# Performance work log

Measured on AMD Instinct MI355X. Metric: run time of the kernel, lower is better.

## Reference

```python
import jax, jax.numpy as jnp
import numpy as np

N = 50000   # nodes
E = 800000  # edges (avg degree 16)
D = 128     # feature dim (in_feats and all hidden_feats)
L = 3       # number of SAGEConv layers


def setup_inputs() -> dict:
    key = jax.random.key(0)
    ks = jax.random.split(key, 3 + 3 * L)
    node_feats = jax.random.normal(ks[0], (N, D), dtype=jnp.float32)
    src = jax.random.randint(ks[1], (E,), 0, N)
    dst = jax.random.randint(ks[2], (E,), 0, N)
    inp = {"node_feats": node_feats, "src": src, "dst": dst}
    scale = 1.0 / np.sqrt(D)
    for i in range(L):
        inp[f"W_self{i}"] = (jax.random.normal(ks[3 + 3 * i], (D, D), dtype=jnp.float32) * scale)
        inp[f"W_neigh{i}"] = (jax.random.normal(ks[4 + 3 * i], (D, D), dtype=jnp.float32) * scale)
        inp[f"b{i}"] = jnp.zeros((D,), dtype=jnp.float32)
    return inp


def _sage_stack(node_feats, src, dst, layers):
    n = node_feats.shape[0]
    # in-degree per destination node, clamped so isolated nodes yield 0 aggregate
    deg = jax.ops.segment_sum(jnp.ones((src.shape[0],), dtype=node_feats.dtype), dst, num_segments=n)
    inv_deg = (1.0 / jnp.maximum(deg, 1.0))[:, None]  # [N,1]
    h = node_feats
    for (W_s, W_n, b) in layers:
        # gather neighbor feats along edges, mean-reduce into dst nodes
        agg = jax.ops.segment_sum(h[src], dst, num_segments=n) * inv_deg  # [N,D]
        # DGL SAGEConv ('mean'): fc_self(h_dst) + fc_neigh(mean_neigh) + bias, then activation
        h = jax.nn.relu(h @ W_s.T + agg @ W_n.T + b)
    return h


def reference(node_feats, src, dst, W_self0, W_neigh0, b0, W_self1, W_neigh1, b1, W_self2, W_neigh2, b2):
    layers = ((W_self0, W_neigh0, b0), (W_self1, W_neigh1, b1), (W_self2, W_neigh2, b2))
    return _sage_stack(node_feats, src, dst, layers)
```

## Files before the change

kernel.cpp:

```cpp
#include <hip/hip_runtime.h>
#include <hip/hip_bf16.h>

#define NN 50000
#define NE 800000
#define DF 128
#define NSL 128
#define SLN 391
#define CAP 8192
#define ECHUNK 1563

typedef __bf16 bf16x8 __attribute__((ext_vector_type(8)));
typedef float f32x4 __attribute__((ext_vector_type(4)));

__device__ __forceinline__ unsigned short f32_to_bf16_rne(float f) {
    unsigned int u = __float_as_uint(f);
    u += 0x7fffu + ((u >> 16) & 1u);
    return (unsigned short)(u >> 16);
}

__device__ __forceinline__ unsigned int pack_bf16x2(float lo, float hi) {
    return (unsigned int)f32_to_bf16_rne(lo) | ((unsigned int)f32_to_bf16_rne(hi) << 16);
}

__global__ __launch_bounds__(256) void k_bucket(const int* __restrict__ src, const int* __restrict__ dst,
                                                int* __restrict__ gcur, uint2* __restrict__ bucket) {
    __shared__ int cnt[NSL];
    __shared__ int rb[NSL];
    int t = threadIdx.x;
    for (int j = t; j < NSL; j += 256) cnt[j] = 0;
    __syncthreads();
    int base = blockIdx.x * ECHUNK;
    int end = base + ECHUNK;
    if (end > NE) end = NE;
    for (int i = base + t; i < end; i += 256) atomicAdd(&cnt[dst[i] / SLN], 1);
    __syncthreads();
    for (int j = t; j < NSL; j += 256) rb[j] = atomicAdd(&gcur[j], cnt[j]);
    __syncthreads();
    for (int j = t; j < NSL; j += 256) cnt[j] = rb[j];
    __syncthreads();
    for (int i = base + t; i < end; i += 256) {
        int d = dst[i];
        int s = d / SLN;
        int pos = atomicAdd(&cnt[s], 1);
        bucket[s * CAP + pos] = make_uint2((unsigned)src[i], (unsigned)d);
    }
}

__global__ void k_sbase(const int* __restrict__ gcur, int* __restrict__ sbase, int* __restrict__ row_ptr) {
    if (threadIdx.x == 0) {
        int acc = 0;
        for (int s = 0; s < NSL; ++s) {
            sbase[s] = acc;
            acc += gcur[s];
        }
        row_ptr[NN] = acc;
    }
}

__global__ __launch_bounds__(256) void k_cslice(const uint2* __restrict__ bucket, const int* __restrict__ gcur,
                                                const int* __restrict__ sbase, int* __restrict__ col,
                                                int* __restrict__ row_ptr, float* __restrict__ inv_deg) {
    __shared__ int sdeg[512];
    __shared__ int scur[512];
    int s = blockIdx.x;
    int t = threadIdx.x;
    int nbase = s * SLN;
    int ncnt = NN - nbase;
    if (ncnt > SLN) ncnt = SLN;
    int ecnt = gcur[s];
    int eb = s * CAP;
    int cb = sbase[s];
    sdeg[t] = 0;
    sdeg[t + 256] = 0;
    __syncthreads();
    for (int e = t; e < ecnt; e += 256) atomicAdd(&sdeg[bucket[eb + e].y - nbase], 1);
    __syncthreads();
    int d0 = sdeg[t], d1 = sdeg[t + 256];
    for (int off = 1; off < 512; off <<= 1) {
        int v0 = (t >= off) ? sdeg[t - off] : 0;
        int v1 = (t + 256 >= off) ? sdeg[t + 256 - off] : 0;
        __syncthreads();
        sdeg[t] += v0;
        sdeg[t + 256] += v1;
        __syncthreads();
    }
    int e0 = sdeg[t] - d0, e1 = sdeg[t + 256] - d1;
    scur[t] = e0;
    scur[t + 256] = e1;
    if (t < ncnt) {
        row_ptr[nbase + t] = cb + e0;
        inv_deg[nbase + t] = 1.0f / (float)(d0 > 1 ? d0 : 1);
    }
    if (t + 256 < ncnt) {
        row_ptr[nbase + t + 256] = cb + e1;
        inv_deg[nbase + t + 256] = 1.0f / (float)(d1 > 1 ? d1 : 1);
    }
    __syncthreads();
    for (int e = t; e < ecnt; e += 256) {
        uint2 pr = bucket[eb + e];
        int p = atomicAdd(&scur[pr.y - nbase], 1);
        col[cb + p] = (int)pr.x;
    }
}

__global__ __launch_bounds__(256) void k_f2b_all(const float* __restrict__ feats,
                                                 const float* __restrict__ w0, const float* __restrict__ w1,
                                                 const float* __restrict__ w2, const float* __restrict__ w3,
                                                 const float* __restrict__ w4, const float* __restrict__ w5,
                                                 unsigned short* __restrict__ h_bf,
                                                 unsigned short* __restrict__ Wb) {
    int i = (blockIdx.x * 256 + threadIdx.x) * 4;
    const float* fsrc;
    unsigned short* dstp;
    if (i < NN * DF) {
        fsrc = feats + i;
        dstp = h_bf + i;
    } else {
        int j = i - NN * DF;
        if (j >= 6 * DF * DF) return;
        int w = j >> 14;
        int o = j & 16383;
        const float* ws[6] = {w0, w1, w2, w3, w4, w5};
        fsrc = ws[w] + o;
        dstp = Wb + w * DF * DF + o;
    }
    float4 v = *reinterpret_cast<const float4*>(fsrc);
    ushort4 r;
    r.x = f32_to_bf16_rne(v.x);
    r.y = f32_to_bf16_rne(v.y);
    r.z = f32_to_bf16_rne(v.z);
    r.w = f32_to_bf16_rne(v.w);
    *reinterpret_cast<ushort4*>(dstp) = r;
}

__global__ __launch_bounds__(256) void k_agg(const unsigned short* __restrict__ H,
                                             const int* __restrict__ row_ptr, const int* __restrict__ col,
                                             const float* __restrict__ inv_deg,
                                             unsigned short* __restrict__ Agg, int n) {
    int wid = threadIdx.x >> 6;
    int lane = threadIdx.x & 63;
    int node = blockIdx.x * 4 + wid;
    if (node >= n) return;
    int s = row_ptr[node], e = row_ptr[node + 1];
    int g = lane >> 4;
    int l = lane & 15;
    int off = l * 8;

    float a[8];
#pragma unroll
    for (int k = 0; k < 8; ++k) a[k] = 0.f;

    for (int j = s; j < e; j += 8) {
        int j0 = j + g;
        int j1 = j + 4 + g;
        if (j0 < e) {
            int c = col[j0];
            uint4 u = *reinterpret_cast<const uint4*>(H + (size_t)c * DF + off);
            a[0] += __uint_as_float(u.x << 16);
            a[1] += __uint_as_float(u.x & 0xffff0000u);
            a[2] += __uint_as_float(u.y << 16);
            a[3] += __uint_as_float(u.y & 0xffff0000u);
            a[4] += __uint_as_float(u.z << 16);
            a[5] += __uint_as_float(u.z & 0xffff0000u);
            a[6] += __uint_as_float(u.w << 16);
            a[7] += __uint_as_float(u.w & 0xffff0000u);
        }
        if (j1 < e) {
            int c = col[j1];
            uint4 u = *reinterpret_cast<const uint4*>(H + (size_t)c * DF + off);
            a[0] += __uint_as_float(u.x << 16);
            a[1] += __uint_as_float(u.x & 0xffff0000u);
            a[2] += __uint_as_float(u.y << 16);
            a[3] += __uint_as_float(u.y & 0xffff0000u);
            a[4] += __uint_as_float(u.z << 16);
            a[5] += __uint_as_float(u.z & 0xffff0000u);
            a[6] += __uint_as_float(u.w << 16);
            a[7] += __uint_as_float(u.w & 0xffff0000u);
        }
    }

#pragma unroll
    for (int k = 0; k < 8; ++k) {
        a[k] += __shfl_xor(a[k], 16, 64);
        a[k] += __shfl_xor(a[k], 32, 64);
    }

    if (g == 0) {
        float iv = inv_deg[node];
        uint4 r;
        r.x = pack_bf16x2(a[0] * iv, a[1] * iv);
        r.y = pack_bf16x2(a[2] * iv, a[3] * iv);
        r.z = pack_bf16x2(a[4] * iv, a[5] * iv);
        r.w = pack_bf16x2(a[6] * iv, a[7] * iv);
        *reinterpret_cast<uint4*>(Agg + (size_t)node * DF + off) = r;
    }
}

__global__ __launch_bounds__(256) void k_gemm(const unsigned short* __restrict__ Hb,
                                              const unsigned short* __restrict__ Ab,
                                              const unsigned short* __restrict__ Wb,
                                              const float* __restrict__ bias,
                                              unsigned short* __restrict__ Hout,
                                              float* __restrict__ Fout,
                                              int n) {
    int brow = blockIdx.x * 64;
    int lane = threadIdx.x & 63;
    int wid = threadIdx.x >> 6;
    int l15 = lane & 15;
    int lk = (lane >> 4) * 8;
    int colb = wid * 32;

    f32x4 zero = {0.f, 0.f, 0.f, 0.f};
    f32x4 acc[4][2];
#pragma unroll
    for (int m = 0; m < 4; ++m) {
        acc[m][0] = zero;
        acc[m][1] = zero;
    }

#pragma unroll
    for (int ph = 0; ph < 2; ++ph) {
        const unsigned short* Ap = ph ? Ab : Hb;
        const unsigned short* Wp = Wb + ph * (DF * DF);
#pragma unroll
        for (int ks = 0; ks < 4; ++ks) {
            int kb = ks * 32 + lk;
            bf16x8 bfr0 = *reinterpret_cast<const bf16x8*>(Wp + (colb + l15) * DF + kb);
            bf16x8 bfr1 = *reinterpret_cast<const bf16x8*>(Wp + (colb + 16 + l15) * DF + kb);
#pragma unroll
            for (int m = 0; m < 4; ++m) {
                int r = brow + m * 16 + l15;
                if (r >= n) r = n - 1;
                bf16x8 afr = *reinterpret_cast<const bf16x8*>(Ap + (size_t)r * DF + kb);
                acc[m][0] = __builtin_amdgcn_mfma_f32_16x16x32_bf16(afr, bfr0, acc[m][0], 0, 0, 0);
                acc[m][1] = __builtin_amdgcn_mfma_f32_16x16x32_bf16(afr, bfr1, acc[m][1], 0, 0, 0);
            }
        }
    }

    __syncthreads();

    int rb = (lane >> 4) * 4;
#pragma unroll
    for (int q = 0; q < 2; ++q) {
        int o = colb + q * 16 + l15;
        float bv = bias[o];
#pragma unroll
        for (int m = 0; m < 4; ++m) {
#pragma unroll
            for (int j = 0; j < 4; ++j) {
                int r = brow + m * 16 + rb + j;
                if (r < n) {
                    float v = fmaxf(acc[m][q][j] + bv, 0.f);
                    if (Fout) Fout[(size_t)r * DF + o] = v;
                    else Hout[(size_t)r * DF + o] = f32_to_bf16_rne(v);
                }
            }
        }
    }
}

extern "C" void kernel_launch(void* const* d_in, const int* in_sizes, int n_in,
                              void* d_out, int out_size, void* d_ws, size_t ws_size,
                              hipStream_t stream) {
    const float* feats = (const float*)d_in[0];
    const int* src = (const int*)d_in[1];
    const int* dst = (const int*)d_in[2];
    const float* bias[3] = {(const float*)d_in[5], (const float*)d_in[8], (const float*)d_in[11]};

    char* ws = (char*)d_ws;
    unsigned short* h_bf = (unsigned short*)(ws);
    unsigned short* agg_bf = (unsigned short*)(ws + 12800000);
    uint2* bucket = (uint2*)(ws + 12800000);
    unsigned short* Wb = (unsigned short*)(ws + 25600000);
    int* row_ptr = (int*)(ws + 25796608);
    float* inv_deg = (float*)(ws + 25996616);
    int* col = (int*)(ws + 26196616);
    int* gcur = (int*)(ws + 29396616);
    int* sbase = (int*)(ws + 29397128);

    hipMemsetAsync(gcur, 0, NSL * sizeof(int), stream);
    k_bucket<<<512, 256, 0, stream>>>(src, dst, gcur, bucket);
    k_sbase<<<1, 64, 0, stream>>>(gcur, sbase, row_ptr);
    k_cslice<<<NSL, 256, 0, stream>>>(bucket, gcur, sbase, col, row_ptr, inv_deg);

    int qtot = (NN * DF + 6 * DF * DF) / 4;
    k_f2b_all<<<(qtot + 255) / 256, 256, 0, stream>>>(
        feats, (const float*)d_in[3], (const float*)d_in[4], (const float*)d_in[6],
        (const float*)d_in[7], (const float*)d_in[9], (const float*)d_in[10], h_bf, Wb);

    int gblk = (NN + 63) / 64;
    for (int l = 0; l < 3; ++l) {
        k_agg<<<(NN + 3) / 4, 256, 0, stream>>>(h_bf, row_ptr, col, inv_deg, agg_bf, NN);
        const unsigned short* Wl = Wb + l * 2 * DF * DF;
        if (l < 2)
            k_gemm<<<gblk, 256, 0, stream>>>(h_bf, agg_bf, Wl, bias[l], h_bf, nullptr, NN);
        else
            k_gemm<<<gblk, 256, 0, stream>>>(h_bf, agg_bf, Wl, bias[l], nullptr, (float*)d_out, NN);
    }
}
```

Baseline: 260.5 us.

## Split neighbor aggregation into four feature-column panels for L2 locality

The aggregation kernel now splits the 128-wide bf16 feature dimension into four 32-column panels. Blocks are ordered panel-major, so all nodes are processed for one panel before the next, and each lane gathers 4 bytes per edge instead of 16. The intent is that the working set of gathered H columns (50000 x 64 bytes per panel) fits in cache and random gathers hit L2/MALL more often. The cost is four times as many blocks, repeated reads of row_ptr and col for every panel, and narrower, less efficient memory transactions.

```diff
diff --git a/kernel.cpp b/kernel.cpp
--- a/kernel.cpp
+++ b/kernel.cpp
@@ -8,6 +8,8 @@
 #define SLN 391
 #define CAP 8192
 #define ECHUNK 1563
+#define NPAN 4
+#define NBLK 12500
 
 typedef __bf16 bf16x8 __attribute__((ext_vector_type(8)));
 typedef float f32x4 __attribute__((ext_vector_type(4)));
@@ -137,62 +139,44 @@
                                              const int* __restrict__ row_ptr, const int* __restrict__ col,
                                              const float* __restrict__ inv_deg,
                                              unsigned short* __restrict__ Agg, int n) {
+    int pb = blockIdx.x / NBLK;
+    int nb = blockIdx.x % NBLK;
     int wid = threadIdx.x >> 6;
     int lane = threadIdx.x & 63;
-    int node = blockIdx.x * 4 + wid;
+    int node = nb * 4 + wid;
     if (node >= n) return;
     int s = row_ptr[node], e = row_ptr[node + 1];
     int g = lane >> 4;
     int l = lane & 15;
-    int off = l * 8;
-
-    float a[8];
-#pragma unroll
-    for (int k = 0; k < 8; ++k) a[k] = 0.f;
+    int off = pb * 32 + l * 2;
+
+    float a0 = 0.f, a1 = 0.f;
 
     for (int j = s; j < e; j += 8) {
         int j0 = j + g;
         int j1 = j + 4 + g;
         if (j0 < e) {
             int c = col[j0];
-            uint4 u = *reinterpret_cast<const uint4*>(H + (size_t)c * DF + off);
-            a[0] += __uint_as_float(u.x << 16);
-            a[1] += __uint_as_float(u.x & 0xffff0000u);
-            a[2] += __uint_as_float(u.y << 16);
-            a[3] += __uint_as_float(u.y & 0xffff0000u);
-            a[4] += __uint_as_float(u.z << 16);
-            a[5] += __uint_as_float(u.z & 0xffff0000u);
-            a[6] += __uint_as_float(u.w << 16);
-            a[7] += __uint_as_float(u.w & 0xffff0000u);
+            unsigned int u = *reinterpret_cast<const unsigned int*>(H + (size_t)c * DF + off);
+            a0 += __uint_as_float(u << 16);
+            a1 += __uint_as_float(u & 0xffff0000u);
         }
         if (j1 < e) {
             int c = col[j1];
-            uint4 u = *reinterpret_cast<const uint4*>(H + (size_t)c * DF + off);
-            a[0] += __uint_as_float(u.x << 16);
-            a[1] += __uint_as_float(u.x & 0xffff0000u);
-            a[2] += __uint_as_float(u.y << 16);
-            a[3] += __uint_as_float(u.y & 0xffff0000u);
-            a[4] += __uint_as_float(u.z << 16);
-            a[5] += __uint_as_float(u.z & 0xffff0000u);
-            a[6] += __uint_as_float(u.w << 16);
-            a[7] += __uint_as_float(u.w & 0xffff0000u);
-        }
-    }
-
-#pragma unroll
-    for (int k = 0; k < 8; ++k) {
-        a[k] += __shfl_xor(a[k], 16, 64);
-        a[k] += __shfl_xor(a[k], 32, 64);
-    }
+            unsigned int u = *reinterpret_cast<const unsigned int*>(H + (size_t)c * DF + off);
+            a0 += __uint_as_float(u << 16);
+            a1 += __uint_as_float(u & 0xffff0000u);
+        }
+    }
+
+    a0 += __shfl_xor(a0, 16, 64);
+    a0 += __shfl_xor(a0, 32, 64);
+    a1 += __shfl_xor(a1, 16, 64);
+    a1 += __shfl_xor(a1, 32, 64);
 
     if (g == 0) {
         float iv = inv_deg[node];
-        uint4 r;
-        r.x = pack_bf16x2(a[0] * iv, a[1] * iv);
-        r.y = pack_bf16x2(a[2] * iv, a[3] * iv);
-        r.z = pack_bf16x2(a[4] * iv, a[5] * iv);
-        r.w = pack_bf16x2(a[6] * iv, a[7] * iv);
-        *reinterpret_cast<uint4*>(Agg + (size_t)node * DF + off) = r;
+        *reinterpret_cast<unsigned int*>(Agg + (size_t)node * DF + off) = pack_bf16x2(a0 * iv, a1 * iv);
     }
 }
 
@@ -291,7 +275,7 @@
 
     int gblk = (NN + 63) / 64;
     for (int l = 0; l < 3; ++l) {
-        k_agg<<<(NN + 3) / 4, 256, 0, stream>>>(h_bf, row_ptr, col, inv_deg, agg_bf, NN);
+        k_agg<<<NPAN * NBLK, 256, 0, stream>>>(h_bf, row_ptr, col, inv_deg, agg_bf, NN);
         const unsigned short* Wl = Wb + l * 2 * DF * DF;
         if (l < 2)
             k_gemm<<<gblk, 256, 0, stream>>>(h_bf, agg_bf, Wl, bias[l], h_bf, nullptr, NN);
```

Measured after the change: 472.4 us. 1.81x slower.
